# Kernel optimization log

Measured on AMD Instinct MI355X. Metric: run time of the kernel, lower is better.

The kernel has to match this reference:

```python
import jax, jax.numpy as jnp
import numpy as np

B, T, C = 8, 2048, 1024
NEG = -1.0e10  # torch fill value -10000000000.0

def setup_inputs() -> dict:
    key = jax.random.key(0)
    k1, k2, k3 = jax.random.split(key, 3)
    return {
        "query": jax.random.normal(k1, (B, T, C), dtype=jnp.float32),
        "keys": jax.random.normal(k2, (B, T, C), dtype=jnp.float32),
        "values": jax.random.normal(k3, (B, T, C), dtype=jnp.float32),
        "mask": jnp.ones((B, T), dtype=jnp.float32),
        "m": 128,
    }

def reference(query, keys, values, mask, m):
    num_tags = query.shape[-1]
    scale = 1.0 / np.sqrt(num_tags).astype(np.float32)
    # energy[b,t,s] = <query[b,t], keys[b,s]>
    energy = jnp.einsum('btc,bsc->bts', query, keys)
    if m > 0:
        idx = jnp.arange(query.shape[1])
        band = jnp.where(jnp.abs(idx[:, None] - idx[None, :]) <= m,
                         jnp.float32(0.0), jnp.float32(NEG))
        energy = energy + band[None, :, :]
    # torch applies scale AFTER adding mask (mul_ after the add), then softmax
    att = jax.nn.softmax(energy * scale, axis=2)
    lc = jnp.einsum('bts,bsc->btc', att, values)
    lc = lc * mask[:, :, None]
    # form == 'max': max over channel dim, then sum over time -> [B]
    return lc.max(axis=2).sum(axis=1)
```

## Files before the change

### kernel.cpp

```cpp
#include <hip/hip_runtime.h>
#include <math.h>

#define T_DIM 2048
#define C_DIM 1024
#define B_DIM 8
#define TB    32
#define KROW  72
#define PROW  296

typedef float f32x4 __attribute__((ext_vector_type(4)));
typedef short s16x8 __attribute__((ext_vector_type(8)));

__device__ __forceinline__ unsigned short f2bf(float x) {
    union { float f; unsigned u; } v; v.f = x;
    unsigned r = v.u + 0x7fffu + ((v.u >> 16) & 1u);
    return (unsigned short)(r >> 16);
}
__device__ __forceinline__ unsigned pk2(float a, float b) {
    return (unsigned)f2bf(a) | ((unsigned)f2bf(b) << 16);
}

__device__ __forceinline__ void gll16(const void* g, void* l) {
    __builtin_amdgcn_global_load_lds(
        (const __attribute__((address_space(1))) unsigned int*)g,
        (__attribute__((address_space(3))) unsigned int*)l,
        16, 0, 0);
}

__global__ __launch_bounds__(256)
void conv_k(const float* __restrict__ X, unsigned short* __restrict__ Xb)
{
    const size_t base = (size_t)blockIdx.y * T_DIM * C_DIM
                      + (size_t)blockIdx.x * 2048 + (size_t)threadIdx.x * 8;
    const float4* src = (const float4*)(X + base);
    float4 x = src[0], y = src[1];
    uint4 o;
    o.x = pk2(x.x, x.y); o.y = pk2(x.z, x.w);
    o.z = pk2(y.x, y.y); o.w = pk2(y.z, y.w);
    *(uint4*)(Xb + base) = o;
}

__global__ __launch_bounds__(256)
void tile_k(const float* __restrict__ K, unsigned short* __restrict__ Kt)
{
    const int tile = blockIdx.x;
    const int b    = blockIdx.y;
    const int tid  = threadIdx.x;
    const int w = tid >> 6, l = tid & 63, g = l >> 4, ln = l & 15;
    const float* src_row = K + (size_t)(b * T_DIM + tile * 16 + ln) * C_DIM;
#pragma unroll
    for (int kki = 0; kki < 8; ++kki) {
        const int kk = kki * 4 + w;
        const float4* p = (const float4*)(src_row + kk * 32 + g * 8);
        float4 x = p[0], y = p[1];
        uint4 o;
        o.x = pk2(x.x, x.y); o.y = pk2(x.z, x.w);
        o.z = pk2(y.x, y.y); o.w = pk2(y.z, y.w);
        *(uint4*)(Kt + (size_t)(((b * 128 + tile) * 32 + kk) * 64 + l) * 8) = o;
    }
}

__global__ __launch_bounds__(256)
void transpose_vx(const float* __restrict__ V, unsigned short* __restrict__ out,
                  int frag_mode)
{
    __shared__ float buf[64 * 67];
    const int t0 = blockIdx.x * 64;
    const int c0 = blockIdx.y * 64;
    const int b  = blockIdx.z;
    const float* Vb = V + (size_t)b * T_DIM * C_DIM;

    for (int i = threadIdx.x; i < 64 * 64; i += 256) {
        const int r = i >> 6, c = i & 63;
        buf[r * 67 + c] = Vb[(size_t)(t0 + r) * C_DIM + c0 + c];
    }
    __syncthreads();
    const int t8 = threadIdx.x & 7;
    const int cl = threadIdx.x >> 3;
#pragma unroll
    for (int half = 0; half < 2; ++half) {
        const int c_loc = cl + half * 32;
        float v[8];
#pragma unroll
        for (int j = 0; j < 8; ++j) v[j] = buf[(t8 * 8 + j) * 67 + c_loc];
        uint4 o;
        o.x = pk2(v[0], v[1]); o.y = pk2(v[2], v[3]);
        o.z = pk2(v[4], v[5]); o.w = pk2(v[6], v[7]);
        if (frag_mode) {
            const int ct = (c0 + c_loc) >> 4, lnv = c_loc & 15;
            const int g = t8 & 3, sg = (t0 >> 5) + (t8 >> 2);
            *(uint4*)(out + (size_t)(((b * 64 + ct) * 64 + sg) * 64 + g * 16 + lnv) * 8) = o;
        } else {
            *(uint4*)(out + (size_t)(b * C_DIM + c0 + c_loc) * T_DIM + t0 + t8 * 8) = o;
        }
    }
}

__global__ __launch_bounds__(256, 2)
void attn_band_tiled(const unsigned short* __restrict__ Qb,
                     const unsigned short* __restrict__ Kt,
                     const unsigned short* __restrict__ Vtt,
                     const float* __restrict__ Mask, const int* __restrict__ m_ptr,
                     float* __restrict__ wsrow)
{
    __shared__ __align__(16) short SMEM[30208];
    __shared__ float pmax[64], psum[64], red[64];
    short* Kbuf = SMEM;
    short* P    = SMEM;
    short* Vbuf = SMEM + 9728;

    const int h = blockIdx.x;
    const int logical = (h & 7) * 64 + (h >> 3);
    const int b  = logical >> 6;
    const int t0 = (logical & 63) * TB;

    const int tid = threadIdx.x;
    const int w = tid >> 6, lane = tid & 63, g = lane >> 4, ln = lane & 15;
    const int th = w >> 1, sh = w & 1;
    const int m  = m_ptr[0];

    const int s_lo = max(0, t0 - m);
    const int s_hi = min(T_DIM - 1, t0 + TB - 1 + m);
    const int sg0  = s_lo >> 5;

    const unsigned short* Qgb = Qb  + (size_t)b * T_DIM * C_DIM;
    const unsigned short* Ktb = Kt  + (size_t)b * 128 * 32 * 512;
    const unsigned short* Vtb = Vtt + (size_t)b * 64 * 64 * 512;

    f32x4 E[9];
    f32x4 zed = {0.f, 0.f, 0.f, 0.f};
#pragma unroll
    for (int i = 0; i < 9; ++i) E[i] = zed;

#define STAGE1(KN, NB)                                                              \
    {                                                                               \
        short* dstb = Kbuf + (NB) * 10240;                                          \
        _Pragma("unroll")                                                           \
        for (int f5 = 0; f5 < 5; ++f5) {                                            \
            const int f = w * 5 + f5;                                               \
            if (f < 18) {                                                           \
                const int ktile = min(sg0 * 2 + f, 127);                            \
                gll16(Ktb + ((size_t)(ktile * 32 + (KN)) * 64 + lane) * 8,          \
                      dstb + f * 512);                                              \
            } else {                                                                \
                const int qt = f - 18;                                              \
                gll16(Qgb + (size_t)(t0 + qt * 16 + ln) * C_DIM + (KN) * 32 + g * 8,\
                      dstb + f * 512);                                              \
            }                                                                       \
        }                                                                           \
    }

    STAGE1(0, 0);
    __syncthreads();

#pragma unroll 2
    for (int kk = 0; kk < 32; ++kk) {
        const int cur = kk & 1;
        if (kk < 31) STAGE1(kk + 1, cur ^ 1);
        const short* cb = Kbuf + cur * 10240;
        s16x8 aq = *(const s16x8*)(cb + (18 + th) * 512 + lane * 8);
#pragma unroll
        for (int i = 0; i < 9; ++i) {
            s16x8 bk = *(const s16x8*)(cb + (sh * 9 + i) * 512 + lane * 8);
            E[i] = __builtin_amdgcn_mfma_f32_16x16x32_bf16(aq, bk, E[i], 0, 0, 0);
        }
        __syncthreads();
    }

    const float scale = 0.03125f;
    const int rowb = th * 16 + g * 4;
    float lm[4];
#pragma unroll
    for (int r = 0; r < 4; ++r) lm[r] = -INFINITY;
    const int s_base = s_lo + sh * 144 + ln;
#pragma unroll
    for (int i = 0; i < 9; ++i) {
        const int s = s_base + i * 16;
#pragma unroll
        for (int r = 0; r < 4; ++r) {
            const int t = t0 + rowb + r;
            int d = t - s; d = d < 0 ? -d : d;
            const bool valid = (s <= s_hi) && (d <= m);
            float e = valid ? E[i][r] : -INFINITY;
            E[i][r] = e;
            lm[r] = fmaxf(lm[r], e);
        }
    }
#pragma unroll
    for (int r = 0; r < 4; ++r)
#pragma unroll
        for (int dd = 1; dd < 16; dd <<= 1) lm[r] = fmaxf(lm[r], __shfl_xor(lm[r], dd));
    if (ln == 0) {
#pragma unroll
        for (int r = 0; r < 4; ++r) pmax[sh * 32 + rowb + r] = lm[r];
    }
    __syncthreads();
    float Mr[4], sum[4];
#pragma unroll
    for (int r = 0; r < 4; ++r) {
        Mr[r] = fmaxf(pmax[rowb + r], pmax[32 + rowb + r]) * scale;
        sum[r] = 0.f;
    }
#pragma unroll
    for (int i = 0; i < 9; ++i)
#pragma unroll
        for (int r = 0; r < 4; ++r) {
            float e = __expf(E[i][r] * scale - Mr[r]);
            E[i][r] = e;
            sum[r] += e;
        }
#pragma unroll
    for (int r = 0; r < 4; ++r)
#pragma unroll
        for (int dd = 1; dd < 16; dd <<= 1) sum[r] += __shfl_xor(sum[r], dd);
    if (ln == 0) {
#pragma unroll
        for (int r = 0; r < 4; ++r) psum[sh * 32 + rowb + r] = sum[r];
    }
    __syncthreads();
    float inv[4];
#pragma unroll
    for (int r = 0; r < 4; ++r) inv[r] = 1.0f / (psum[rowb + r] + psum[32 + rowb + r]);
#pragma unroll
    for (int i = 0; i < 9; ++i) {
        const int col = sh * 144 + i * 16 + ln;
#pragma unroll
        for (int r = 0; r < 4; ++r)
            P[(rowb + r) * PROW + col] = (short)f2bf(E[i][r] * inv[r]);
    }
    __syncthreads();

    s16x8 pa[9];
#pragma unroll
    for (int kg = 0; kg < 9; ++kg)
        pa[kg] = *(const s16x8*)(P + (th * 16 + ln) * PROW + kg * 32 + g * 8);

    int sgc[9];
#pragma unroll
    for (int kg = 0; kg < 9; ++kg) sgc[kg] = min(sg0 + kg, 63);

    float maskv[4], rmax[4];
#pragma unroll
    for (int r = 0; r < 4; ++r) {
        maskv[r] = Mask[(size_t)b * T_DIM + t0 + rowb + r];
        rmax[r]  = -INFINITY;
    }

#define STAGE3(S, NB)                                                               \
    {                                                                               \
        const int q_ = (S) >> 1;                                                    \
        short* dstb = Vbuf + (NB) * 10240;                                          \
        const int ct_ = q_ * 4 + w;                                                 \
        if (((S) & 1) == 0) {                                                       \
            _Pragma("unroll")                                                       \
            for (int e = 0; e < 5; ++e)                                             \
                gll16(Vtb + ((size_t)(ct_ * 64 + sgc[e]) * 64 + lane) * 8,          \
                      dstb + (w * 5 + e) * 512);                                    \
        } else {                                                                    \
            _Pragma("unroll")                                                       \
            for (int e = 0; e < 4; ++e)                                             \
                gll16(Vtb + ((size_t)(ct_ * 64 + sgc[5 + e]) * 64 + lane) * 8,      \
                      dstb + (w * 4 + e) * 512);                                    \
        }                                                                           \
    }

    STAGE3(0, 0);
    __syncthreads();

    f32x4 O0 = zed, O1 = zed;
#pragma unroll 2
    for (int s = 0; s < 32; ++s) {
        const int cur = s & 1;
        if (s < 31) STAGE3(s + 1, cur ^ 1);
        const short* vb = Vbuf + cur * 10240;
        if ((s & 1) == 0) {
            O0 = zed; O1 = zed;
#pragma unroll
            for (int e = 0; e < 5; ++e) {
                s16x8 bv0 = *(const s16x8*)(vb + ((sh * 2    ) * 5 + e) * 512 + lane * 8);
                s16x8 bv1 = *(const s16x8*)(vb + ((sh * 2 + 1) * 5 + e) * 512 + lane * 8);
                O0 = __builtin_amdgcn_mfma_f32_16x16x32_bf16(pa[e], bv0, O0, 0, 0, 0);
                O1 = __builtin_amdgcn_mfma_f32_16x16x32_bf16(pa[e], bv1, O1, 0, 0, 0);
            }
        } else {
#pragma unroll
            for (int e = 0; e < 4; ++e) {
                s16x8 bv0 = *(const s16x8*)(vb + ((sh * 2    ) * 4 + e) * 512 + lane * 8);
                s16x8 bv1 = *(const s16x8*)(vb + ((sh * 2 + 1) * 4 + e) * 512 + lane * 8);
                O0 = __builtin_amdgcn_mfma_f32_16x16x32_bf16(pa[5 + e], bv0, O0, 0, 0, 0);
                O1 = __builtin_amdgcn_mfma_f32_16x16x32_bf16(pa[5 + e], bv1, O1, 0, 0, 0);
            }
#pragma unroll
            for (int r = 0; r < 4; ++r) {
                rmax[r] = fmaxf(rmax[r], O0[r] * maskv[r]);
                rmax[r] = fmaxf(rmax[r], O1[r] * maskv[r]);
            }
        }
        __syncthreads();
    }

#pragma unroll
    for (int r = 0; r < 4; ++r)
#pragma unroll
        for (int dd = 1; dd < 16; dd <<= 1) rmax[r] = fmaxf(rmax[r], __shfl_xor(rmax[r], dd));
    if (ln == 0) {
#pragma unroll
        for (int r = 0; r < 4; ++r) red[sh * 32 + rowb + r] = rmax[r];
    }
    __syncthreads();
    if (tid < 32)
        wsrow[(size_t)b * T_DIM + t0 + tid] = fmaxf(red[tid], red[32 + tid]);
}

__global__ __launch_bounds__(256, 2)
void attn_band_mfma(const float* __restrict__ Q, const float* __restrict__ K,
                    const unsigned short* __restrict__ Vt,
                    const float* __restrict__ Mask, const int* __restrict__ m_ptr,
                    float* __restrict__ wsrow)
{
    __shared__ __align__(16) char smem_raw[57600];
    short* SM = (short*)smem_raw;
    short* Kc = SM;
    short* Qc = SM + 288 * KROW;
    short* P  = SM;
    short* Vl = SM + 32 * PROW;
    float* pmax = (float*)(smem_raw + 56832);
    float* psum = pmax + 64;
    float* red  = psum + 64;

    const int h = blockIdx.x;
    const int logical = (h & 7) * 64 + (h >> 3);
    const int b  = logical >> 6;
    const int t0 = (logical & 63) * TB;

    const int tid = threadIdx.x;
    const int w = tid >> 6, lane = tid & 63, g = lane >> 4, ln = lane & 15;
    const int th = w >> 1, sh = w & 1;
    const int m  = m_ptr[0];

    const int s_lo = max(0, t0 - m);
    const int s_hi = min(T_DIM - 1, t0 + TB - 1 + m);

    const float* Qb = Q + (size_t)b * T_DIM * C_DIM;
    const float* Kb = K + (size_t)b * T_DIM * C_DIM;
    const unsigned short* Vtb = Vt + (size_t)b * C_DIM * T_DIM;

    f32x4 E[9];
    f32x4 zed = {0.f, 0.f, 0.f, 0.f};
#pragma unroll
    for (int i = 0; i < 9; ++i) E[i] = zed;

    for (int cc = 0; cc < C_DIM / 64; ++cc) {
        const int c0 = cc * 64;
        __syncthreads();
        for (int u = tid; u < 288 * 8; u += 256) {
            const int su = u >> 3, un = u & 7;
            const int s = min(s_lo + su, T_DIM - 1);
            const float4* src = (const float4*)(Kb + (size_t)s * C_DIM + c0 + un * 8);
            float4 x = src[0], y = src[1];
            uint4 o; o.x = pk2(x.x, x.y); o.y = pk2(x.z, x.w);
            o.z = pk2(y.x, y.y); o.w = pk2(y.z, y.w);
            *(uint4*)(Kc + su * KROW + un * 8) = o;
        }
        {
            const int su = tid >> 3, un = tid & 7;
            const float4* src = (const float4*)(Qb + (size_t)(t0 + su) * C_DIM + c0 + un * 8);
            float4 x = src[0], y = src[1];
            uint4 o; o.x = pk2(x.x, x.y); o.y = pk2(x.z, x.w);
            o.z = pk2(y.x, y.y); o.w = pk2(y.z, y.w);
            *(uint4*)(Qc + su * KROW + un * 8) = o;
        }
        __syncthreads();
        s16x8 aq[2];
#pragma unroll
        for (int kk = 0; kk < 2; ++kk)
            aq[kk] = *(const s16x8*)(Qc + (th * 16 + ln) * KROW + kk * 32 + g * 8);
#pragma unroll
        for (int i = 0; i < 9; ++i) {
            const int srow2 = (sh * 9 + i) * 16 + ln;
#pragma unroll
            for (int kk = 0; kk < 2; ++kk) {
                s16x8 bk = *(const s16x8*)(Kc + srow2 * KROW + kk * 32 + g * 8);
                E[i] = __builtin_amdgcn_mfma_f32_16x16x32_bf16(aq[kk], bk, E[i], 0, 0, 0);
            }
        }
    }

    const float scale = 0.03125f;
    const int rowb = th * 16 + g * 4;
    float lm[4];
#pragma unroll
    for (int r = 0; r < 4; ++r) lm[r] = -INFINITY;
    const int s_base = s_lo + sh * 144 + ln;
#pragma unroll
    for (int i = 0; i < 9; ++i) {
        const int s = s_base + i * 16;
#pragma unroll
        for (int r = 0; r < 4; ++r) {
            const int t = t0 + rowb + r;
            int d = t - s; d = d < 0 ? -d : d;
            const bool valid = (s <= s_hi) && (d <= m);
            float e = valid ? E[i][r] : -INFINITY;
            E[i][r] = e;
            lm[r] = fmaxf(lm[r], e);
        }
    }
#pragma unroll
    for (int r = 0; r < 4; ++r)
#pragma unroll
        for (int dd = 1; dd < 16; dd <<= 1) lm[r] = fmaxf(lm[r], __shfl_xor(lm[r], dd));
    if (ln == 0) {
#pragma unroll
        for (int r = 0; r < 4; ++r) pmax[sh * 32 + rowb + r] = lm[r];
    }
    __syncthreads();
    float Mr[4], sum[4];
#pragma unroll
    for (int r = 0; r < 4; ++r) {
        Mr[r] = fmaxf(pmax[rowb + r], pmax[32 + rowb + r]) * scale;
        sum[r] = 0.f;
    }
#pragma unroll
    for (int i = 0; i < 9; ++i)
#pragma unroll
        for (int r = 0; r < 4; ++r) {
            float e = __expf(E[i][r] * scale - Mr[r]);
            E[i][r] = e;
            sum[r] += e;
        }
#pragma unroll
    for (int r = 0; r < 4; ++r)
#pragma unroll
        for (int dd = 1; dd < 16; dd <<= 1) sum[r] += __shfl_xor(sum[r], dd);
    if (ln == 0) {
#pragma unroll
        for (int r = 0; r < 4; ++r) psum[sh * 32 + rowb + r] = sum[r];
    }
    __syncthreads();
    float inv[4];
#pragma unroll
    for (int r = 0; r < 4; ++r) inv[r] = 1.0f / (psum[rowb + r] + psum[32 + rowb + r]);
#pragma unroll
    for (int i = 0; i < 9; ++i) {
        const int col = sh * 144 + i * 16 + ln;
#pragma unroll
        for (int r = 0; r < 4; ++r)
            P[(rowb + r) * PROW + col] = (short)f2bf(E[i][r] * inv[r]);
    }
    __syncthreads();

    s16x8 pa[9];
#pragma unroll
    for (int kg = 0; kg < 9; ++kg)
        pa[kg] = *(const s16x8*)(P + (th * 16 + ln) * PROW + kg * 32 + g * 8);

    float maskv[4], rmax[4];
#pragma unroll
    for (int r = 0; r < 4; ++r) {
        maskv[r] = Mask[(size_t)b * T_DIM + t0 + rowb + r];
        rmax[r]  = -INFINITY;
    }

    for (int cc = 0; cc < C_DIM / 64; ++cc) {
        __syncthreads();
        for (int i2 = tid; i2 < 64 * 36; i2 += 256) {
            const int cr = i2 / 36, un = i2 - cr * 36;
            const int sb = min(s_lo + un * 8, T_DIM - 8);
            uint4 x = *(const uint4*)(Vtb + (size_t)(cc * 64 + cr) * T_DIM + sb);
            *(uint4*)(Vl + cr * PROW + un * 8) = x;
        }
        __syncthreads();
#pragma unroll
        for (int nbi = 0; nbi < 2; ++nbi) {
            const int crow = sh * 32 + nbi * 16 + ln;
            f32x4 O = zed;
#pragma unroll
            for (int kg = 0; kg < 9; ++kg) {
                s16x8 bv = *(const s16x8*)(Vl + crow * PROW + kg * 32 + g * 8);
                O = __builtin_amdgcn_mfma_f32_16x16x32_bf16(pa[kg], bv, O, 0, 0, 0);
            }
#pragma unroll
            for (int r = 0; r < 4; ++r)
                rmax[r] = fmaxf(rmax[r], O[r] * maskv[r]);
        }
    }
#pragma unroll
    for (int r = 0; r < 4; ++r)
#pragma unroll
        for (int dd = 1; dd < 16; dd <<= 1) rmax[r] = fmaxf(rmax[r], __shfl_xor(rmax[r], dd));
    if (ln == 0) {
#pragma unroll
        for (int r = 0; r < 4; ++r) red[sh * 32 + rowb + r] = rmax[r];
    }
    __syncthreads();
    if (tid < 32)
        wsrow[(size_t)b * T_DIM + t0 + tid] = fmaxf(red[tid], red[32 + tid]);
}

__global__ void reduce_b(const float* __restrict__ ws, float* __restrict__ out)
{
    const int b = blockIdx.x;
    float s = 0.f;
    for (int t = threadIdx.x; t < T_DIM; t += 256) s += ws[(size_t)b * T_DIM + t];
#pragma unroll
    for (int dd = 32; dd > 0; dd >>= 1) s += __shfl_xor(s, dd);
    __shared__ float acc[4];
    if ((threadIdx.x & 63) == 0) acc[threadIdx.x >> 6] = s;
    __syncthreads();
    if (threadIdx.x == 0) out[b] = acc[0] + acc[1] + acc[2] + acc[3];
}

extern "C" void kernel_launch(void* const* d_in, const int* in_sizes, int n_in,
                              void* d_out, int out_size, void* d_ws, size_t ws_size,
                              hipStream_t stream)
{
    const float* Q    = (const float*)d_in[0];
    const float* K    = (const float*)d_in[1];
    const float* V    = (const float*)d_in[2];
    const float* Mask = (const float*)d_in[3];
    const int*   m    = (const int*)d_in[4];
    float* out = (float*)d_out;

    const size_t frag_bytes = (size_t)B_DIM * T_DIM * C_DIM * 2;
    const size_t need_main  = 3 * frag_bytes + (size_t)B_DIM * T_DIM * 4;
    const size_t need_fb    = frag_bytes + (size_t)B_DIM * T_DIM * 4;

    if (ws_size >= need_main) {
        unsigned short* Qb  = (unsigned short*)d_ws;
        unsigned short* Kt  = (unsigned short*)((char*)d_ws + frag_bytes);
        unsigned short* Vtt = (unsigned short*)((char*)d_ws + 2 * frag_bytes);
        float* wsrow = (float*)((char*)d_ws + 3 * frag_bytes);
        conv_k<<<dim3(1024, B_DIM), 256, 0, stream>>>(Q, Qb);
        tile_k<<<dim3(128, B_DIM), 256, 0, stream>>>(K, Kt);
        transpose_vx<<<dim3(T_DIM / 64, C_DIM / 64, B_DIM), 256, 0, stream>>>(V, Vtt, 1);
        attn_band_tiled<<<dim3((T_DIM / TB) * B_DIM), 256, 0, stream>>>(Qb, Kt, Vtt, Mask, m, wsrow);
        reduce_b<<<B_DIM, 256, 0, stream>>>(wsrow, out);
    } else {
        unsigned short* Vt = (unsigned short*)d_ws;
        float* wsrow = (float*)((char*)d_ws + frag_bytes);
        transpose_vx<<<dim3(T_DIM / 64, C_DIM / 64, B_DIM), 256, 0, stream>>>(V, Vt, 0);
        attn_band_mfma<<<dim3((T_DIM / TB) * B_DIM), 256, 0, stream>>>(Q, K, Vt, Mask, m, wsrow);
        reduce_b<<<B_DIM, 256, 0, stream>>>(wsrow, out);
    }
}
```

Baseline: 112.6 us.

## Fuse Q bf16 conversion into attention kernel and hold Q fragments in registers

Removes the separate Q-to-bf16 conversion kernel and its workspace buffer. The attention kernel now loads fp32 Q rows directly, converts them to bf16 and keeps all 32 k-slice fragments in registers, while LDS staging carries only K tiles. This avoids an extra global write and read of the converted Q and one kernel launch. In exchange it raises register pressure with 128 extra VGPRs and fully unrolls the K loop, which risks spills or a long up-front load latency.

```diff
diff --git a/kernel.cpp b/kernel.cpp
--- a/kernel.cpp
+++ b/kernel.cpp
@@ -25,19 +25,6 @@
         (const __attribute__((address_space(1))) unsigned int*)g,
         (__attribute__((address_space(3))) unsigned int*)l,
         16, 0, 0);
-}
-
-__global__ __launch_bounds__(256)
-void conv_k(const float* __restrict__ X, unsigned short* __restrict__ Xb)
-{
-    const size_t base = (size_t)blockIdx.y * T_DIM * C_DIM
-                      + (size_t)blockIdx.x * 2048 + (size_t)threadIdx.x * 8;
-    const float4* src = (const float4*)(X + base);
-    float4 x = src[0], y = src[1];
-    uint4 o;
-    o.x = pk2(x.x, x.y); o.y = pk2(x.z, x.w);
-    o.z = pk2(y.x, y.y); o.w = pk2(y.z, y.w);
-    *(uint4*)(Xb + base) = o;
 }
 
 __global__ __launch_bounds__(256)
@@ -97,7 +84,7 @@
 }
 
 __global__ __launch_bounds__(256, 2)
-void attn_band_tiled(const unsigned short* __restrict__ Qb,
+void attn_band_tiled(const float* __restrict__ Qf,
                      const unsigned short* __restrict__ Kt,
                      const unsigned short* __restrict__ Vtt,
                      const float* __restrict__ Mask, const int* __restrict__ m_ptr,
@@ -123,46 +110,52 @@
     const int s_hi = min(T_DIM - 1, t0 + TB - 1 + m);
     const int sg0  = s_lo >> 5;
 
-    const unsigned short* Qgb = Qb  + (size_t)b * T_DIM * C_DIM;
     const unsigned short* Ktb = Kt  + (size_t)b * 128 * 32 * 512;
     const unsigned short* Vtb = Vtt + (size_t)b * 64 * 64 * 512;
 
+    s16x8 aqr[32];
+    {
+        const float* qrow = Qf + (size_t)(b * T_DIM + t0 + th * 16 + ln) * C_DIM;
+#pragma unroll
+        for (int kk = 0; kk < 32; ++kk) {
+            const float4* qp = (const float4*)(qrow + kk * 32 + g * 8);
+            float4 qx = qp[0], qy = qp[1];
+            uint4 a;
+            a.x = pk2(qx.x, qx.y); a.y = pk2(qx.z, qx.w);
+            a.z = pk2(qy.x, qy.y); a.w = pk2(qy.z, qy.w);
+            aqr[kk] = *(s16x8*)&a;
+        }
+    }
+
     f32x4 E[9];
     f32x4 zed = {0.f, 0.f, 0.f, 0.f};
 #pragma unroll
     for (int i = 0; i < 9; ++i) E[i] = zed;
 
-#define STAGE1(KN, NB)                                                              \
+#define STAGE1K(KN, NB)                                                             \
     {                                                                               \
-        short* dstb = Kbuf + (NB) * 10240;                                          \
+        short* dstb = Kbuf + (NB) * 9216;                                           \
         _Pragma("unroll")                                                           \
         for (int f5 = 0; f5 < 5; ++f5) {                                            \
             const int f = w * 5 + f5;                                               \
-            if (f < 18) {                                                           \
-                const int ktile = min(sg0 * 2 + f, 127);                            \
-                gll16(Ktb + ((size_t)(ktile * 32 + (KN)) * 64 + lane) * 8,          \
+            if (f < 18)                                                             \
+                gll16(Ktb + ((size_t)(min(sg0 * 2 + f, 127) * 32 + (KN)) * 64 + lane) * 8, \
                       dstb + f * 512);                                              \
-            } else {                                                                \
-                const int qt = f - 18;                                              \
-                gll16(Qgb + (size_t)(t0 + qt * 16 + ln) * C_DIM + (KN) * 32 + g * 8,\
-                      dstb + f * 512);                                              \
-            }                                                                       \
         }                                                                           \
     }
 
-    STAGE1(0, 0);
-    __syncthreads();
-
-#pragma unroll 2
+    STAGE1K(0, 0);
+    __syncthreads();
+
+#pragma unroll
     for (int kk = 0; kk < 32; ++kk) {
         const int cur = kk & 1;
-        if (kk < 31) STAGE1(kk + 1, cur ^ 1);
-        const short* cb = Kbuf + cur * 10240;
-        s16x8 aq = *(const s16x8*)(cb + (18 + th) * 512 + lane * 8);
+        if (kk < 31) STAGE1K(kk + 1, cur ^ 1);
+        const short* cb = Kbuf + cur * 9216;
 #pragma unroll
         for (int i = 0; i < 9; ++i) {
             s16x8 bk = *(const s16x8*)(cb + (sh * 9 + i) * 512 + lane * 8);
-            E[i] = __builtin_amdgcn_mfma_f32_16x16x32_bf16(aq, bk, E[i], 0, 0, 0);
+            E[i] = __builtin_amdgcn_mfma_f32_16x16x32_bf16(aqr[kk], bk, E[i], 0, 0, 0);
         }
         __syncthreads();
     }
@@ -522,18 +515,15 @@
     float* out = (float*)d_out;
 
     const size_t frag_bytes = (size_t)B_DIM * T_DIM * C_DIM * 2;
-    const size_t need_main  = 3 * frag_bytes + (size_t)B_DIM * T_DIM * 4;
-    const size_t need_fb    = frag_bytes + (size_t)B_DIM * T_DIM * 4;
+    const size_t need_main  = 2 * frag_bytes + (size_t)B_DIM * T_DIM * 4;
 
     if (ws_size >= need_main) {
-        unsigned short* Qb  = (unsigned short*)d_ws;
-        unsigned short* Kt  = (unsigned short*)((char*)d_ws + frag_bytes);
-        unsigned short* Vtt = (unsigned short*)((char*)d_ws + 2 * frag_bytes);
-        float* wsrow = (float*)((char*)d_ws + 3 * frag_bytes);
-        conv_k<<<dim3(1024, B_DIM), 256, 0, stream>>>(Q, Qb);
+        unsigned short* Kt  = (unsigned short*)d_ws;
+        unsigned short* Vtt = (unsigned short*)((char*)d_ws + frag_bytes);
+        float* wsrow = (float*)((char*)d_ws + 2 * frag_bytes);
         tile_k<<<dim3(128, B_DIM), 256, 0, stream>>>(K, Kt);
         transpose_vx<<<dim3(T_DIM / 64, C_DIM / 64, B_DIM), 256, 0, stream>>>(V, Vtt, 1);
-        attn_band_tiled<<<dim3((T_DIM / TB) * B_DIM), 256, 0, stream>>>(Qb, Kt, Vtt, Mask, m, wsrow);
+        attn_band_tiled<<<dim3((T_DIM / TB) * B_DIM), 256, 0, stream>>>(Q, Kt, Vtt, Mask, m, wsrow);
         reduce_b<<<B_DIM, 256, 0, stream>>>(wsrow, out);
     } else {
         unsigned short* Vt = (unsigned short*)d_ws;
```

New measurement: 150.3 us. 33.5% more time.
